# Performance work log

Measured on AMD Instinct MI355X. Metric: run time of the kernel, lower is better.

The kernel has to match this reference:

```python
import jax, jax.numpy as jnp
import numpy as np

N, K, C, SP = 65536, 16, 64, 8
C8 = C // SP  # attn_nn output dim == C // share_planes == 8
E = N * K
EPS = 1e-5


def _bn(x, g, b):
    # BatchNorm1d in training mode: batch statistics over the row dim
    mu = x.mean(0)
    var = ((x - mu) ** 2).mean(0)
    return (x - mu) * jax.lax.rsqrt(var + EPS) * g + b


def _segment_softmax(a, seg, n):
    m = jax.ops.segment_max(a, seg, num_segments=n)
    e = jnp.exp(a - m[seg])
    s = jax.ops.segment_sum(e, seg, num_segments=n)
    return e / s[seg]


def setup_inputs() -> dict:
    key = jax.random.key(0)
    ks = jax.random.split(key, 12)

    def w(k, shape, fan_in):
        return jax.random.normal(k, shape, jnp.float32) / np.sqrt(fan_in).astype(np.float32)

    x = jax.random.normal(ks[0], (N, C), jnp.float32)
    pos = jax.random.uniform(ks[1], (N, 3), jnp.float32)
    src = jax.random.randint(ks[2], (E,), 0, N)          # knn neighbor ids
    dst = jnp.repeat(jnp.arange(N), K)                   # k neighbors per target node
    edge_index = jnp.stack([src, dst]).astype(jnp.int32)
    return dict(
        x=x, pos=pos, edge_index=edge_index,
        W_in=w(ks[3], (C, C), C), W_out=w(ks[4], (C, C), C),
        pos_w1=w(ks[5], (3, 3), 3), pos_b1=jnp.zeros(3, jnp.float32),
        pos_bn_g=jnp.ones(3, jnp.float32), pos_bn_b=jnp.zeros(3, jnp.float32),
        pos_w2=w(ks[6], (C, 3), 3), pos_b2=jnp.zeros(C, jnp.float32),
        attn_bn1_g=jnp.ones(C, jnp.float32), attn_bn1_b=jnp.zeros(C, jnp.float32),
        attn_w1=w(ks[7], (C8, C), C), attn_b1=jnp.zeros(C8, jnp.float32),
        attn_bn2_g=jnp.ones(C8, jnp.float32), attn_bn2_b=jnp.zeros(C8, jnp.float32),
        attn_w2=w(ks[8], (C8, C8), C8), attn_b2=jnp.zeros(C8, jnp.float32),
        lin_w=w(ks[9], (C, C), C), lin_b=jnp.zeros(C, jnp.float32),
        src_w=w(ks[10], (C, C), C), src_b=jnp.zeros(C, jnp.float32),
        dst_w=w(ks[11], (C, C), C), dst_b=jnp.zeros(C, jnp.float32),
        bn1_g=jnp.ones(C, jnp.float32), bn1_b=jnp.zeros(C, jnp.float32),
        bn2_g=jnp.ones(C, jnp.float32), bn2_b=jnp.zeros(C, jnp.float32),
        bn3_g=jnp.ones(C, jnp.float32), bn3_b=jnp.zeros(C, jnp.float32),
    )


def reference(x, pos, edge_index, W_in, W_out, pos_w1, pos_b1, pos_bn_g, pos_bn_b,
              pos_w2, pos_b2, attn_bn1_g, attn_bn1_b, attn_w1, attn_b1,
              attn_bn2_g, attn_bn2_b, attn_w2, attn_b2, lin_w, lin_b,
              src_w, src_b, dst_w, dst_b, bn1_g, bn1_b, bn2_g, bn2_b, bn3_g, bn3_b):
    src, dst = edge_index[0], edge_index[1]
    x_skip = x
    # lin_in + bn1 + relu
    h = jax.nn.relu(_bn(x @ W_in.T, bn1_g, bn1_b))

    # --- PointTransformerConv ---
    a_src = h @ src_w.T + src_b
    a_dst = h @ dst_w.T + dst_b
    hW = h @ lin_w.T + lin_b

    rel = pos[src] - pos[dst]              # pos_j - pos_i  [E,3]
    d = jax.nn.relu(_bn(rel @ pos_w1.T + pos_b1, pos_bn_g, pos_bn_b))
    delta = d @ pos_w2.T + pos_b2          # [E,C]

    a = a_src[src] - a_dst[dst] + delta    # alpha_j - alpha_i + delta  [E,C]
    # attn_nn: BN -> ReLU -> (Lin C->C8, BN, ReLU) -> Lin C8->C8
    a = jax.nn.relu(_bn(a, attn_bn1_g, attn_bn1_b))
    a = jax.nn.relu(_bn(a @ attn_w1.T + attn_b1, attn_bn2_g, attn_bn2_b))
    a = a @ attn_w2.T + attn_b2            # [E,C8]
    alpha = _segment_softmax(a, dst, N)    # softmax over each node's neighborhood

    # grouped weighting with share_planes: [E,SP,C8] * [E,1,C8]
    msg = (alpha[:, None, :] * (hW[src] + delta).reshape(E, SP, C8)).reshape(E, C)
    out = jax.ops.segment_sum(msg, dst, num_segments=N)  # aggr='add'

    h2 = jax.nn.relu(_bn(out, bn2_g, bn2_b))
    h3 = _bn(h2 @ W_out.T, bn3_g, bn3_b)
    return jax.nn.relu(h3 + x_skip)
```

## Files before the change

### kernel.cpp

```cpp
#include <hip/hip_runtime.h>
#include <cstddef>

constexpr int N_ = 65536;
constexpr int K_ = 16;
constexpr int E_ = N_ * K_;
constexpr int C_ = 64;
#define EPS_ 1e-5f
#define SW 68
#define INV_N (1.f / 65536.f)
#define INV_E (1.f / 1048576.f)
#define NSLOT 64

typedef unsigned int uint_t;

__device__ __forceinline__ uint_t bf16_rne(float f) {
    uint_t u = __float_as_uint(f);
    return (u + 0x7fffu + ((u >> 16) & 1u)) >> 16;
}
__device__ __forceinline__ float bf16_lo(uint_t p) { return __uint_as_float(p << 16); }
__device__ __forceinline__ float bf16_hi(uint_t p) { return __uint_as_float(p & 0xffff0000u); }

__device__ __forceinline__ void bn_ss(const float* __restrict__ s, int nchp, int c,
                                      float invM, const float* __restrict__ g,
                                      const float* __restrict__ b,
                                      float& sc, float& sh)
{
    float mean = s[c] * invM;
    float var  = fmaxf(s[nchp + c] * invM - mean * mean, 0.f);
    sc = g[c] * rsqrtf(var + EPS_);
    sh = b[c] - mean * sc;
}

__global__ void k_zero(float* __restrict__ p, int n)
{
    int i = blockIdx.x * 1024 + threadIdx.x;
    if (i < n) p[i] = 0.f;
}

__device__ __forceinline__ void stage_x(const float* __restrict__ in,
                                        const float* __restrict__ ss,
                                        float* __restrict__ Xs, int row0, int t)
{
#pragma unroll
    for (int it = 0; it < 4; ++it) {
        int m = t + 256 * it;
        int r = m >> 4, j = m & 15;
        float4 v = ((const float4*)in)[(size_t)(row0 + r) * 16 + j];
        if (ss) {
            float4 sc = ((const float4*)ss)[j];
            float4 sh = ((const float4*)(ss + 64))[j];
            v.x = fmaxf(fmaf(v.x, sc.x, sh.x), 0.f);
            v.y = fmaxf(fmaf(v.y, sc.y, sh.y), 0.f);
            v.z = fmaxf(fmaf(v.z, sc.z, sh.z), 0.f);
            v.w = fmaxf(fmaf(v.w, sc.w, sh.w), 0.f);
        }
        *(float4*)&Xs[r * SW + 4 * j] = v;
    }
}

__device__ __forceinline__ void stage_w(const float* __restrict__ W,
                                        float* __restrict__ Ws, int t)
{
#pragma unroll
    for (int it = 0; it < 4; ++it) {
        int m = t + 256 * it;
        int r = m >> 4, j = m & 15;
        *(float4*)&Ws[r * SW + 4 * j] = ((const float4*)W)[m];
    }
}

__device__ __forceinline__ void compute_tile(const float* __restrict__ Xs,
                                             const float* __restrict__ Ws,
                                             int tx, int ty, float acc[4][4])
{
#pragma unroll
    for (int r = 0; r < 4; ++r)
#pragma unroll
        for (int c = 0; c < 4; ++c) acc[r][c] = 0.f;
    for (int kc = 0; kc < 16; ++kc) {
        float4 xf[4], wf[4];
#pragma unroll
        for (int r = 0; r < 4; ++r)
            xf[r] = *(const float4*)&Xs[(tx + 16 * r) * SW + 4 * kc];
#pragma unroll
        for (int c = 0; c < 4; ++c)
            wf[c] = *(const float4*)&Ws[(ty + 16 * c) * SW + 4 * kc];
#pragma unroll
        for (int r = 0; r < 4; ++r)
#pragma unroll
            for (int c = 0; c < 4; ++c) {
                acc[r][c] = fmaf(xf[r].x, wf[c].x, acc[r][c]);
                acc[r][c] = fmaf(xf[r].y, wf[c].y, acc[r][c]);
                acc[r][c] = fmaf(xf[r].z, wf[c].z, acc[r][c]);
                acc[r][c] = fmaf(xf[r].w, wf[c].w, acc[r][c]);
            }
    }
}

__device__ __forceinline__ void write_tile(float* __restrict__ buf, int tx, int ty,
                                           const float acc[4][4],
                                           const float* __restrict__ bias,
                                           float* __restrict__ out, int row0, int t)
{
    __syncthreads();
#pragma unroll
    for (int r = 0; r < 4; ++r)
#pragma unroll
        for (int c = 0; c < 4; ++c)
            buf[(tx + 16 * r) * SW + ty + 16 * c] = acc[r][c];
    __syncthreads();
#pragma unroll
    for (int it = 0; it < 4; ++it) {
        int m = t + 256 * it;
        int r = m >> 4, j = m & 15;
        float4 v = *(const float4*)&buf[r * SW + 4 * j];
        if (bias) {
            float4 bv = ((const float4*)bias)[j];
            v.x += bv.x; v.y += bv.y; v.z += bv.z; v.w += bv.w;
        }
        ((float4*)out)[(size_t)(row0 + r) * 16 + j] = v;
    }
    __syncthreads();
}

__device__ __forceinline__ void write_tile_bf16(float* __restrict__ buf, int tx, int ty,
                                                const float acc[4][4],
                                                const float* __restrict__ bias,
                                                unsigned short* __restrict__ out,
                                                int row0, int t)
{
    __syncthreads();
#pragma unroll
    for (int r = 0; r < 4; ++r)
#pragma unroll
        for (int c = 0; c < 4; ++c)
            buf[(tx + 16 * r) * SW + ty + 16 * c] = acc[r][c];
    __syncthreads();
#pragma unroll
    for (int it = 0; it < 4; ++it) {
        int m = t + 256 * it;
        int r = m >> 4, j = m & 15;
        float4 v = *(const float4*)&buf[r * SW + 4 * j];
        if (bias) {
            float4 bv = ((const float4*)bias)[j];
            v.x += bv.x; v.y += bv.y; v.z += bv.z; v.w += bv.w;
        }
        uint2 o;
        o.x = bf16_rne(v.x) | (bf16_rne(v.y) << 16);
        o.y = bf16_rne(v.z) | (bf16_rne(v.w) << 16);
        ((uint2*)out)[(size_t)(row0 + r) * 16 + j] = o;
    }
    __syncthreads();
}

__global__ __launch_bounds__(256)
void k_gemm_tile(const float* __restrict__ in, const float* __restrict__ W,
                 const float* __restrict__ acc_in, const float* __restrict__ g_in,
                 const float* __restrict__ b_in, float invM_in,
                 float* __restrict__ out, float* __restrict__ acc_out)
{
    __shared__ float Xs[64 * SW];
    __shared__ float Ws[64 * SW];
    __shared__ float ssm[128];
    __shared__ float raws[128];
    int t = threadIdx.x, tx = t & 15, ty = t >> 4;
    int row0 = blockIdx.x * 64;
    if (acc_in) {
        if (t < 128) {
            float s = 0.f;
            for (int sl = 0; sl < NSLOT; ++sl) s += acc_in[sl * 128 + t];
            raws[t] = s;
        }
        __syncthreads();
        if (t < 64) {
            float scv, shv;
            bn_ss(raws, 64, t, invM_in, g_in, b_in, scv, shv);
            ssm[t] = scv; ssm[64 + t] = shv;
        }
    }
    __syncthreads();
    stage_x(in, acc_in ? ssm : nullptr, Xs, row0, t);
    stage_w(W, Ws, t);
    __syncthreads();
    float acc[4][4];
    compute_tile(Xs, Ws, tx, ty, acc);
    __syncthreads();
#pragma unroll
    for (int r = 0; r < 4; ++r)
#pragma unroll
        for (int c = 0; c < 4; ++c)
            Ws[(tx + 16 * r) * SW + ty + 16 * c] = acc[r][c];
    __syncthreads();
    float s0 = 0, s1 = 0, s2 = 0, s3 = 0, q0 = 0, q1 = 0, q2 = 0, q3 = 0;
#pragma unroll
    for (int it = 0; it < 4; ++it) {
        int m = t + 256 * it;
        int r = m >> 4, j = m & 15;
        float4 v = *(const float4*)&Ws[r * SW + 4 * j];
        ((float4*)out)[(size_t)(row0 + r) * 16 + j] = v;
        s0 += v.x; q0 = fmaf(v.x, v.x, q0);
        s1 += v.y; q1 = fmaf(v.y, v.y, q1);
        s2 += v.z; q2 = fmaf(v.z, v.z, q2);
        s3 += v.w; q3 = fmaf(v.w, v.w, q3);
    }
    float4* scr = (float4*)Xs;
    scr[t]       = make_float4(s0, s1, s2, s3);
    scr[256 + t] = make_float4(q0, q1, q2, q3);
    __syncthreads();
    if (t < 16) {
        float4 S = make_float4(0, 0, 0, 0), Q = make_float4(0, 0, 0, 0);
#pragma unroll
        for (int k = 0; k < 16; ++k) {
            float4 a = scr[k * 16 + t], b = scr[256 + k * 16 + t];
            S.x += a.x; S.y += a.y; S.z += a.z; S.w += a.w;
            Q.x += b.x; Q.y += b.y; Q.z += b.z; Q.w += b.w;
        }
        float* ao = acc_out + (blockIdx.x & (NSLOT - 1)) * 128;
        atomicAdd(&ao[4 * t + 0], S.x); atomicAdd(&ao[4 * t + 1], S.y);
        atomicAdd(&ao[4 * t + 2], S.z); atomicAdd(&ao[4 * t + 3], S.w);
        atomicAdd(&ao[64 + 4 * t + 0], Q.x); atomicAdd(&ao[64 + 4 * t + 1], Q.y);
        atomicAdd(&ao[64 + 4 * t + 2], Q.z); atomicAdd(&ao[64 + 4 * t + 3], Q.w);
    }
}

__global__ __launch_bounds__(256)
void k_gemm3_tile(const float* __restrict__ y, const float* __restrict__ acc1,
                  const float* __restrict__ g1, const float* __restrict__ b1,
                  const float* __restrict__ Wa, const float* __restrict__ ba,
                  const float* __restrict__ Wb, const float* __restrict__ bb,
                  const float* __restrict__ Wc, const float* __restrict__ bc,
                  unsigned short* __restrict__ oa16, float* __restrict__ ob,
                  unsigned short* __restrict__ oc16)
{
    __shared__ float Xs[64 * SW];
    __shared__ float Ws[64 * SW];
    __shared__ float ssm[128];
    __shared__ float raws[128];
    int t = threadIdx.x, tx = t & 15, ty = t >> 4;
    int row0 = blockIdx.x * 64;
    if (t < 128) {
        float s = 0.f;
        for (int sl = 0; sl < NSLOT; ++sl) s += acc1[sl * 128 + t];
        raws[t] = s;
    }
    __syncthreads();
    if (t < 64) {
        float scv, shv;
        bn_ss(raws, 64, t, INV_N, g1, b1, scv, shv);
        ssm[t] = scv; ssm[64 + t] = shv;
    }
    __syncthreads();
    stage_x(y, ssm, Xs, row0, t);
    stage_w(Wa, Ws, t);
    __syncthreads();
    float acc[4][4];
    compute_tile(Xs, Ws, tx, ty, acc);
    write_tile_bf16(Ws, tx, ty, acc, ba, oa16, row0, t);
    stage_w(Wb, Ws, t);
    __syncthreads();
    compute_tile(Xs, Ws, tx, ty, acc);
    write_tile(Ws, tx, ty, acc, bb, ob, row0, t);
    stage_w(Wc, Ws, t);
    __syncthreads();
    compute_tile(Xs, Ws, tx, ty, acc);
    write_tile_bf16(Ws, tx, ty, acc, bc, oc16, row0, t);
}

__global__ __launch_bounds__(256)
void k_pos_stats(const float* __restrict__ pos, const int* __restrict__ src,
                 const float* __restrict__ pw1, const float* __restrict__ pb1,
                 float* __restrict__ acc)
{
    float s0 = 0, s1 = 0, s2 = 0, q0 = 0, q1 = 0, q2 = 0;
    int tid = blockIdx.x * 256 + threadIdx.x;
    for (int e = tid; e < E_; e += 1024 * 256) {
        int si = src[e], di = e >> 4;
        float rx = pos[3 * si + 0] - pos[3 * di + 0];
        float ry = pos[3 * si + 1] - pos[3 * di + 1];
        float rz = pos[3 * si + 2] - pos[3 * di + 2];
        float u0 = fmaf(rx, pw1[0], fmaf(ry, pw1[1], fmaf(rz, pw1[2], pb1[0])));
        float u1 = fmaf(rx, pw1[3], fmaf(ry, pw1[4], fmaf(rz, pw1[5], pb1[1])));
        float u2 = fmaf(rx, pw1[6], fmaf(ry, pw1[7], fmaf(rz, pw1[8], pb1[2])));
        s0 += u0; q0 = fmaf(u0, u0, q0);
        s1 += u1; q1 = fmaf(u1, u1, q1);
        s2 += u2; q2 = fmaf(u2, u2, q2);
    }
#pragma unroll
    for (int m = 1; m < 64; m <<= 1) {
        s0 += __shfl_xor(s0, m, 64); s1 += __shfl_xor(s1, m, 64); s2 += __shfl_xor(s2, m, 64);
        q0 += __shfl_xor(q0, m, 64); q1 += __shfl_xor(q1, m, 64); q2 += __shfl_xor(q2, m, 64);
    }
    __shared__ float red[4][8];
    int wv = threadIdx.x >> 6, ln = threadIdx.x & 63;
    if (ln == 0) {
        red[wv][0] = s0; red[wv][1] = s1; red[wv][2] = s2; red[wv][3] = 0.f;
        red[wv][4] = q0; red[wv][5] = q1; red[wv][6] = q2; red[wv][7] = 0.f;
    }
    __syncthreads();
    if (threadIdx.x < 8)
        atomicAdd(&acc[(blockIdx.x & (NSLOT - 1)) * 32 + threadIdx.x],
                  red[0][threadIdx.x] + red[1][threadIdx.x] + red[2][threadIdx.x] + red[3][threadIdx.x]);
}

__global__ __launch_bounds__(256)
void k_abn1_stats(const float* __restrict__ pos, const int* __restrict__ src,
                  const unsigned short* __restrict__ asrc16,
                  const float* __restrict__ adst,
                  const float* __restrict__ pw1, const float* __restrict__ pb1,
                  const float* __restrict__ accpos, const float* __restrict__ pbg,
                  const float* __restrict__ pbb, const float* __restrict__ pw2,
                  const float* __restrict__ pb2, float* __restrict__ acc_a1)
{
    __shared__ float rawP[8];
    int t = threadIdx.x;
    int l = t & 15, g = t >> 4, wv = t >> 6;
    int c0 = 4 * l;
    if (t < 8) {
        float s = 0.f;
        for (int sl = 0; sl < NSLOT; ++sl) s += accpos[sl * 32 + t];
        rawP[t] = s;
    }
    __syncthreads();
    float ps0, ph0, ps1, ph1, ps2, ph2;
    bn_ss(rawP, 4, 0, INV_E, pbg, pbb, ps0, ph0);
    bn_ss(rawP, 4, 1, INV_E, pbg, pbb, ps1, ph1);
    bn_ss(rawP, 4, 2, INV_E, pbg, pbb, ps2, ph2);
    float4 p0 = *(const float4*)(pw2 + 12 * l);
    float4 p1 = *(const float4*)(pw2 + 12 * l + 4);
    float4 p2 = *(const float4*)(pw2 + 12 * l + 8);
    float4 pb = *(const float4*)(pb2 + c0);
    float sa0 = 0, sa1 = 0, sa2 = 0, sa3 = 0;
    float qa0 = 0, qa1 = 0, qa2 = 0, qa3 = 0;
#pragma unroll
    for (int nn = 0; nn < 2; ++nn) {
        int n = blockIdx.x * 32 + nn * 16 + g;
        float4 dv = *(const float4*)(adst + (size_t)n * 64 + c0);
        float pnx = pos[3 * n + 0], pny = pos[3 * n + 1], pnz = pos[3 * n + 2];
        int si_l = src[n * 16 + l];
        float rx = pos[3 * si_l + 0] - pnx;
        float ry = pos[3 * si_l + 1] - pny;
        float rz = pos[3 * si_l + 2] - pnz;
        float u0 = fmaf(rx, pw1[0], fmaf(ry, pw1[1], fmaf(rz, pw1[2], pb1[0])));
        float u1 = fmaf(rx, pw1[3], fmaf(ry, pw1[4], fmaf(rz, pw1[5], pb1[1])));
        float u2 = fmaf(rx, pw1[6], fmaf(ry, pw1[7], fmaf(rz, pw1[8], pb1[2])));
        float dl0 = fmaxf(fmaf(u0, ps0, ph0), 0.f);
        float dl1 = fmaxf(fmaf(u1, ps1, ph1), 0.f);
        float dl2 = fmaxf(fmaf(u2, ps2, ph2), 0.f);
        for (int k = 0; k < 16; ++k) {
            int si = __shfl(si_l, k, 16);
            float d0 = __shfl(dl0, k, 16);
            float d1 = __shfl(dl1, k, 16);
            float d2 = __shfl(dl2, k, 16);
            uint2 raw = ((const uint2*)asrc16)[(size_t)si * 16 + l];
            float avx = bf16_lo(raw.x), avy = bf16_hi(raw.x);
            float avz = bf16_lo(raw.y), avw = bf16_hi(raw.y);
            float del0 = fmaf(d0, p0.x, fmaf(d1, p0.y, fmaf(d2, p0.z, pb.x)));
            float del1 = fmaf(d0, p0.w, fmaf(d1, p1.x, fmaf(d2, p1.y, pb.y)));
            float del2 = fmaf(d0, p1.z, fmaf(d1, p1.w, fmaf(d2, p2.x, pb.z)));
            float del3 = fmaf(d0, p2.y, fmaf(d1, p2.z, fmaf(d2, p2.w, pb.w)));
            float a0 = avx - dv.x + del0;
            float a1 = avy - dv.y + del1;
            float a2 = avz - dv.z + del2;
            float a3 = avw - dv.w + del3;
            sa0 += a0; qa0 = fmaf(a0, a0, qa0);
            sa1 += a1; qa1 = fmaf(a1, a1, qa1);
            sa2 += a2; qa2 = fmaf(a2, a2, qa2);
            sa3 += a3; qa3 = fmaf(a3, a3, qa3);
        }
    }
#pragma unroll
    for (int m = 16; m <= 32; m <<= 1) {
        sa0 += __shfl_xor(sa0, m, 64); sa1 += __shfl_xor(sa1, m, 64);
        sa2 += __shfl_xor(sa2, m, 64); sa3 += __shfl_xor(sa3, m, 64);
        qa0 += __shfl_xor(qa0, m, 64); qa1 += __shfl_xor(qa1, m, 64);
        qa2 += __shfl_xor(qa2, m, 64); qa3 += __shfl_xor(qa3, m, 64);
    }
    __shared__ float red[4][128];
    if ((t & 63) < 16) {
        red[wv][c0 + 0] = sa0; red[wv][c0 + 1] = sa1;
        red[wv][c0 + 2] = sa2; red[wv][c0 + 3] = sa3;
        red[wv][64 + c0 + 0] = qa0; red[wv][64 + c0 + 1] = qa1;
        red[wv][64 + c0 + 2] = qa2; red[wv][64 + c0 + 3] = qa3;
    }
    __syncthreads();
    if (t < 128)
        atomicAdd(&acc_a1[(blockIdx.x & (NSLOT - 1)) * 128 + t],
                  red[0][t] + red[1][t] + red[2][t] + red[3][t]);
}

__global__ __launch_bounds__(256)
void k_edge_t1(const float* __restrict__ pos, const int* __restrict__ src,
               const unsigned short* __restrict__ asrc16,
               const float* __restrict__ adst,
               const float* __restrict__ pw1, const float* __restrict__ pb1,
               const float* __restrict__ accpos, const float* __restrict__ pbg,
               const float* __restrict__ pbb, const float* __restrict__ pw2,
               const float* __restrict__ pb2, const float* __restrict__ acc_a1,
               const float* __restrict__ a1g, const float* __restrict__ a1b,
               const float* __restrict__ aw1, const float* __restrict__ ab1,
               float* __restrict__ t1, float* __restrict__ acc_a2)
{
    __shared__ float rawA1[128];
    __shared__ float rawP[8];
    int t = threadIdx.x;
    int l = t & 15, g = t >> 4, wv = t >> 6;
    int c0 = 4 * l;
    int ch = 4 * (l & 1) + 2 * ((l >> 1) & 1) + ((l >> 2) & 1);
    float abv = ab1[ch];
    if (t < 128) {
        float s = 0.f;
        for (int sl = 0; sl < NSLOT; ++sl) s += acc_a1[sl * 128 + t];
        rawA1[t] = s;
    } else if (t < 136) {
        int i = t - 128;
        float s = 0.f;
        for (int sl = 0; sl < NSLOT; ++sl) s += accpos[sl * 32 + i];
        rawP[i] = s;
    }
    __syncthreads();
    float ps0, ph0, ps1, ph1, ps2, ph2;
    bn_ss(rawP, 4, 0, INV_E, pbg, pbb, ps0, ph0);
    bn_ss(rawP, 4, 1, INV_E, pbg, pbb, ps1, ph1);
    bn_ss(rawP, 4, 2, INV_E, pbg, pbb, ps2, ph2);
    float scx, shx, scy, shy, scz, shz, scw, shw;
    bn_ss(rawA1, 64, c0 + 0, INV_E, a1g, a1b, scx, shx);
    bn_ss(rawA1, 64, c0 + 1, INV_E, a1g, a1b, scy, shy);
    bn_ss(rawA1, 64, c0 + 2, INV_E, a1g, a1b, scz, shz);
    bn_ss(rawA1, 64, c0 + 3, INV_E, a1g, a1b, scw, shw);
    float4 p0 = *(const float4*)(pw2 + 12 * l);
    float4 p1 = *(const float4*)(pw2 + 12 * l + 4);
    float4 p2 = *(const float4*)(pw2 + 12 * l + 8);
    float4 pb = *(const float4*)(pb2 + c0);
    float4 w1[8];
#pragma unroll
    for (int jj = 0; jj < 8; ++jj) w1[jj] = *(const float4*)(aw1 + jj * 64 + c0);
    float sse = 0.f, ssq = 0.f;
#pragma unroll
    for (int nn = 0; nn < 2; ++nn) {
        int n = blockIdx.x * 32 + nn * 16 + g;
        float4 dv = *(const float4*)(adst + (size_t)n * 64 + c0);
        float pnx = pos[3 * n + 0], pny = pos[3 * n + 1], pnz = pos[3 * n + 2];
        int si_l = src[n * 16 + l];
        float rx = pos[3 * si_l + 0] - pnx;
        float ry = pos[3 * si_l + 1] - pny;
        float rz = pos[3 * si_l + 2] - pnz;
        float u0 = fmaf(rx, pw1[0], fmaf(ry, pw1[1], fmaf(rz, pw1[2], pb1[0])));
        float u1 = fmaf(rx, pw1[3], fmaf(ry, pw1[4], fmaf(rz, pw1[5], pb1[1])));
        float u2 = fmaf(rx, pw1[6], fmaf(ry, pw1[7], fmaf(rz, pw1[8], pb1[2])));
        float dl0 = fmaxf(fmaf(u0, ps0, ph0), 0.f);
        float dl1 = fmaxf(fmaf(u1, ps1, ph1), 0.f);
        float dl2 = fmaxf(fmaf(u2, ps2, ph2), 0.f);
        for (int k = 0; k < 16; ++k) {
            int si = __shfl(si_l, k, 16);
            float d0 = __shfl(dl0, k, 16);
            float d1 = __shfl(dl1, k, 16);
            float d2 = __shfl(dl2, k, 16);
            uint2 raw = ((const uint2*)asrc16)[(size_t)si * 16 + l];
            float avx = bf16_lo(raw.x), avy = bf16_hi(raw.x);
            float avz = bf16_lo(raw.y), avw = bf16_hi(raw.y);
            float del0 = fmaf(d0, p0.x, fmaf(d1, p0.y, fmaf(d2, p0.z, pb.x)));
            float del1 = fmaf(d0, p0.w, fmaf(d1, p1.x, fmaf(d2, p1.y, pb.y)));
            float del2 = fmaf(d0, p1.z, fmaf(d1, p1.w, fmaf(d2, p2.x, pb.z)));
            float del3 = fmaf(d0, p2.y, fmaf(d1, p2.z, fmaf(d2, p2.w, pb.w)));
            float an0 = fmaxf(fmaf(avx - dv.x + del0, scx, shx), 0.f);
            float an1 = fmaxf(fmaf(avy - dv.y + del1, scy, shy), 0.f);
            float an2 = fmaxf(fmaf(avz - dv.z + del2, scz, shz), 0.f);
            float an3 = fmaxf(fmaf(avw - dv.w + del3, scw, shw), 0.f);
            float tp[8];
#pragma unroll
            for (int jj = 0; jj < 8; ++jj)
                tp[jj] = fmaf(an0, w1[jj].x, fmaf(an1, w1[jj].y,
                         fmaf(an2, w1[jj].z, an3 * w1[jj].w)));
            float s4[4];
#pragma unroll
            for (int j = 0; j < 4; ++j) {
                float send = (l & 1) ? tp[j] : tp[j + 4];
                float recv = __shfl_xor(send, 1, 64);
                s4[j] = ((l & 1) ? tp[j + 4] : tp[j]) + recv;
            }
            float s2[2];
#pragma unroll
            for (int j = 0; j < 2; ++j) {
                float send = (l & 2) ? s4[j] : s4[j + 2];
                float recv = __shfl_xor(send, 2, 64);
                s2[j] = ((l & 2) ? s4[j + 2] : s4[j]) + recv;
            }
            float send = (l & 4) ? s2[0] : s2[1];
            float recv = __shfl_xor(send, 4, 64);
            float s1 = ((l & 4) ? s2[1] : s2[0]) + recv;
            s1 += __shfl_xor(s1, 8, 64);
            float o = s1 + abv;
            if (l < 8) t1[(size_t)(n * 16 + k) * 8 + ch] = o;
            sse += o; ssq = fmaf(o, o, ssq);
        }
    }
#pragma unroll
    for (int m = 16; m <= 32; m <<= 1) {
        sse += __shfl_xor(sse, m, 64);
        ssq += __shfl_xor(ssq, m, 64);
    }
    __shared__ float red[4][16];
    if ((t & 63) < 8) { red[wv][ch] = sse; red[wv][8 + ch] = ssq; }
    __syncthreads();
    if (t < 16)
        atomicAdd(&acc_a2[(blockIdx.x & (NSLOT - 1)) * 32 + t],
                  red[0][t] + red[1][t] + red[2][t] + red[3][t]);
}

__global__ __launch_bounds__(256)
void k_node_aggr(const float* __restrict__ pos, const int* __restrict__ src,
                 const float* __restrict__ t1, const float* __restrict__ acc_a2,
                 const float* __restrict__ a2g, const float* __restrict__ a2b,
                 const float* __restrict__ aw2, const float* __restrict__ ab2,
                 const unsigned short* __restrict__ hw16,
                 const float* __restrict__ accpos, const float* __restrict__ pbg,
                 const float* __restrict__ pbb,
                 const float* __restrict__ pw1, const float* __restrict__ pb1,
                 const float* __restrict__ pw2, const float* __restrict__ pb2,
                 float* __restrict__ out, float* __restrict__ acc_bn2)
{
    __shared__ float alds[16][196];
    __shared__ float ssm2[16];
    __shared__ float rawA2[16];
    __shared__ float rawP[8];
    int t = threadIdx.x, l = t & 15, g = t >> 4;
    int c0 = 4 * l;
    if (t < 16) {
        float s = 0.f;
        for (int sl = 0; sl < NSLOT; ++sl) s += acc_a2[sl * 32 + t];
        rawA2[t] = s;
    } else if (t < 24) {
        int i = t - 16;
        float s = 0.f;
        for (int sl = 0; sl < NSLOT; ++sl) s += accpos[sl * 32 + i];
        rawP[i] = s;
    }
    __syncthreads();
    if (t < 8) {
        float scv, shv;
        bn_ss(rawA2, 8, t, INV_E, a2g, a2b, scv, shv);
        ssm2[t] = scv; ssm2[8 + t] = shv;
    }
    __syncthreads();
    float ps0, ph0, ps1, ph1, ps2, ph2;
    bn_ss(rawP, 4, 0, INV_E, pbg, pbb, ps0, ph0);
    bn_ss(rawP, 4, 1, INV_E, pbg, pbb, ps1, ph1);
    bn_ss(rawP, 4, 2, INV_E, pbg, pbb, ps2, ph2);
    float4 p0 = *(const float4*)(pw2 + 12 * l);
    float4 p1 = *(const float4*)(pw2 + 12 * l + 4);
    float4 p2 = *(const float4*)(pw2 + 12 * l + 8);
    float4 pb = *(const float4*)(pb2 + c0);
    int alof = (l & 1) * 4;
    int n = blockIdx.x * 16 + g;
    int e = n * 16 + l;
    const float4* t4 = (const float4*)(t1 + (size_t)e * 8);
    float4 ta = t4[0], tb = t4[1];
    float tv[8] = {ta.x, ta.y, ta.z, ta.w, tb.x, tb.y, tb.z, tb.w};
    float tn[8];
#pragma unroll
    for (int j = 0; j < 8; ++j)
        tn[j] = fmaxf(fmaf(tv[j], ssm2[j], ssm2[8 + j]), 0.f);
    float al[8];
#pragma unroll
    for (int j = 0; j < 8; ++j) {
        float acc = ab2[j];
#pragma unroll
        for (int i = 0; i < 8; ++i) acc = fmaf(tn[i], aw2[j * 8 + i], acc);
        float m = acc;
#pragma unroll
        for (int msk = 1; msk < 16; msk <<= 1) m = fmaxf(m, __shfl_xor(m, msk, 64));
        float ex = __expf(acc - m);
        float sm = ex;
#pragma unroll
        for (int msk = 1; msk < 16; msk <<= 1) sm += __shfl_xor(sm, msk, 64);
        al[j] = ex / sm;
    }
    *(float4*)&alds[g][l * 12]     = make_float4(al[0], al[1], al[2], al[3]);
    *(float4*)&alds[g][l * 12 + 4] = make_float4(al[4], al[5], al[6], al[7]);
    int silane = src[e];
    float pnx = pos[3 * n + 0], pny = pos[3 * n + 1], pnz = pos[3 * n + 2];
    float rx = pos[3 * silane + 0] - pnx;
    float ry = pos[3 * silane + 1] - pny;
    float rz = pos[3 * silane + 2] - pnz;
    float u0 = fmaf(rx, pw1[0], fmaf(ry, pw1[1], fmaf(rz, pw1[2], pb1[0])));
    float u1 = fmaf(rx, pw1[3], fmaf(ry, pw1[4], fmaf(rz, pw1[5], pb1[1])));
    float u2 = fmaf(rx, pw1[6], fmaf(ry, pw1[7], fmaf(rz, pw1[8], pb1[2])));
    float dl0 = fmaxf(fmaf(u0, ps0, ph0), 0.f);
    float dl1 = fmaxf(fmaf(u1, ps1, ph1), 0.f);
    float dl2 = fmaxf(fmaf(u2, ps2, ph2), 0.f);
    float a0 = 0.f, a1 = 0.f, a2 = 0.f, a3 = 0.f;
#pragma unroll 4
    for (int k = 0; k < 16; ++k) {
        int sk = __shfl(silane, k, 16);
        float d0 = __shfl(dl0, k, 16);
        float d1 = __shfl(dl1, k, 16);
        float d2 = __shfl(dl2, k, 16);
        uint2 raw = ((const uint2*)hw16)[(size_t)sk * 16 + l];
        float hvx = bf16_lo(raw.x), hvy = bf16_hi(raw.x);
        float hvz = bf16_lo(raw.y), hvw = bf16_hi(raw.y);
        float4 alv = *(const float4*)&alds[g][k * 12 + alof];
        float del0 = fmaf(d0, p0.x, fmaf(d1, p0.y, fmaf(d2, p0.z, pb.x)));
        float del1 = fmaf(d0, p0.w, fmaf(d1, p1.x, fmaf(d2, p1.y, pb.y)));
        float del2 = fmaf(d0, p1.z, fmaf(d1, p1.w, fmaf(d2, p2.x, pb.z)));
        float del3 = fmaf(d0, p2.y, fmaf(d1, p2.z, fmaf(d2, p2.w, pb.w)));
        a0 = fmaf(alv.x, hvx + del0, a0);
        a1 = fmaf(alv.y, hvy + del1, a1);
        a2 = fmaf(alv.z, hvz + del2, a2);
        a3 = fmaf(alv.w, hvw + del3, a3);
    }
    *(float4*)(out + (size_t)n * 64 + c0) = make_float4(a0, a1, a2, a3);
    __syncthreads();
    float4* scr = (float4*)&alds[0][0];
    scr[g * 16 + l]       = make_float4(a0, a1, a2, a3);
    scr[256 + g * 16 + l] = make_float4(a0 * a0, a1 * a1, a2 * a2, a3 * a3);
    __syncthreads();
    if (t < 16) {
        float4 S = make_float4(0, 0, 0, 0), Q = make_float4(0, 0, 0, 0);
#pragma unroll
        for (int k = 0; k < 16; ++k) {
            float4 a = scr[k * 16 + t], b = scr[256 + k * 16 + t];
            S.x += a.x; S.y += a.y; S.z += a.z; S.w += a.w;
            Q.x += b.x; Q.y += b.y; Q.z += b.z; Q.w += b.w;
        }
        float* ao = acc_bn2 + (blockIdx.x & (NSLOT - 1)) * 128;
        atomicAdd(&ao[4 * t + 0], S.x); atomicAdd(&ao[4 * t + 1], S.y);
        atomicAdd(&ao[4 * t + 2], S.z); atomicAdd(&ao[4 * t + 3], S.w);
        atomicAdd(&ao[64 + 4 * t + 0], Q.x); atomicAdd(&ao[64 + 4 * t + 1], Q.y);
        atomicAdd(&ao[64 + 4 * t + 2], Q.z); atomicAdd(&ao[64 + 4 * t + 3], Q.w);
    }
}

__global__ __launch_bounds__(256)
void k_final(const float* __restrict__ y3, const float* __restrict__ acc3,
             const float* __restrict__ g3, const float* __restrict__ b3,
             const float* __restrict__ x, float* __restrict__ out)
{
    __shared__ float raws[128];
    __shared__ float ssl[128];
    int t = threadIdx.x;
    if (t < 128) {
        float s = 0.f;
        for (int sl = 0; sl < NSLOT; ++sl) s += acc3[sl * 128 + t];
        raws[t] = s;
    }
    __syncthreads();
    if (t < 64) {
        float scv, shv;
        bn_ss(raws, 64, t, INV_N, g3, b3, scv, shv);
        ssl[t] = scv; ssl[64 + t] = shv;
    }
    __syncthreads();
    int i = blockIdx.x * 256 + t;
    int c4 = i & 15;
    float4 sc = *(const float4*)&ssl[4 * c4];
    float4 sh = *(const float4*)&ssl[64 + 4 * c4];
    float4 v  = ((const float4*)y3)[i];
    float4 xs = ((const float4*)x)[i];
    float4 o;
    o.x = fmaxf(fmaf(v.x, sc.x, sh.x) + xs.x, 0.f);
    o.y = fmaxf(fmaf(v.y, sc.y, sh.y) + xs.y, 0.f);
    o.z = fmaxf(fmaf(v.z, sc.z, sh.z) + xs.z, 0.f);
    o.w = fmaxf(fmaf(v.w, sc.w, sh.w) + xs.w, 0.f);
    ((float4*)out)[i] = o;
}

extern "C" void kernel_launch(void* const* d_in, const int* in_sizes, int n_in,
                              void* d_out, int out_size, void* d_ws, size_t ws_size,
                              hipStream_t stream)
{
    const float* x    = (const float*)d_in[0];
    const float* pos  = (const float*)d_in[1];
    const int*   src  = (const int*)d_in[2];
    const float* W_in = (const float*)d_in[3];
    const float* W_out= (const float*)d_in[4];
    const float* pw1  = (const float*)d_in[5];
    const float* pb1  = (const float*)d_in[6];
    const float* pbg  = (const float*)d_in[7];
    const float* pbb  = (const float*)d_in[8];
    const float* pw2  = (const float*)d_in[9];
    const float* pb2  = (const float*)d_in[10];
    const float* a1g  = (const float*)d_in[11];
    const float* a1b  = (const float*)d_in[12];
    const float* aw1  = (const float*)d_in[13];
    const float* ab1  = (const float*)d_in[14];
    const float* a2g  = (const float*)d_in[15];
    const float* a2b  = (const float*)d_in[16];
    const float* aw2  = (const float*)d_in[17];
    const float* ab2  = (const float*)d_in[18];
    const float* linw = (const float*)d_in[19];
    const float* linb = (const float*)d_in[20];
    const float* srcw = (const float*)d_in[21];
    const float* srcb = (const float*)d_in[22];
    const float* dstw = (const float*)d_in[23];
    const float* dstb = (const float*)d_in[24];
    const float* bn1g = (const float*)d_in[25];
    const float* bn1b = (const float*)d_in[26];
    const float* bn2g = (const float*)d_in[27];
    const float* bn2b = (const float*)d_in[28];
    const float* bn3g = (const float*)d_in[29];
    const float* bn3b = (const float*)d_in[30];
    float* outp = (float*)d_out;

    float* ws = (float*)d_ws;
    const size_t NC = (size_t)N_ * C_;
    float* buf_y     = ws;
    float* buf_adst  = ws + NC;
    unsigned short* asrc16 = (unsigned short*)(ws + 2 * NC);
    unsigned short* hw16   = (unsigned short*)(ws + 2 * NC + NC / 2);
    float* buf_t1    = ws + 3 * NC;
    float* accb      = ws + 3 * NC + (size_t)E_ * 8;
    float* acc_bn1 = accb;
    float* acc_pos = accb + 64 * 128;
    float* acc_a1  = acc_pos + 64 * 32;
    float* acc_a2  = acc_a1 + 64 * 128;
    float* acc_bn2 = acc_a2 + 64 * 32;
    float* acc_bn3 = acc_bn2 + 64 * 128;
    const int ACC_TOTAL = 64 * (128 + 32 + 128 + 32 + 128 + 128);
    float* buf_out = buf_adst;

    k_zero<<<(ACC_TOTAL + 1023) / 1024, 1024, 0, stream>>>(accb, ACC_TOTAL);
    k_gemm_tile<<<1024, 256, 0, stream>>>(x, W_in, nullptr, nullptr, nullptr, 0.f,
                                          buf_y, acc_bn1);
    k_gemm3_tile<<<1024, 256, 0, stream>>>(buf_y, acc_bn1, bn1g, bn1b,
                                           srcw, srcb, dstw, dstb, linw, linb,
                                           asrc16, buf_adst, hw16);
    k_pos_stats<<<1024, 256, 0, stream>>>(pos, src, pw1, pb1, acc_pos);
    k_abn1_stats<<<2048, 256, 0, stream>>>(pos, src, asrc16, buf_adst,
                                           pw1, pb1, acc_pos, pbg, pbb,
                                           pw2, pb2, acc_a1);
    k_edge_t1<<<2048, 256, 0, stream>>>(pos, src, asrc16, buf_adst,
                                        pw1, pb1, acc_pos, pbg, pbb, pw2, pb2,
                                        acc_a1, a1g, a1b, aw1, ab1,
                                        buf_t1, acc_a2);
    k_node_aggr<<<4096, 256, 0, stream>>>(pos, src, buf_t1, acc_a2, a2g, a2b,
                                          aw2, ab2, hw16, acc_pos, pbg, pbb,
                                          pw1, pb1, pw2, pb2, buf_out, acc_bn2);
    k_gemm_tile<<<1024, 256, 0, stream>>>(buf_out, W_out, acc_bn2, bn2g, bn2b, INV_N,
                                          buf_y, acc_bn3);
    k_final<<<(N_ * C_ / 4) / 256, 256, 0, stream>>>(buf_y, acc_bn3, bn3g, bn3b, x, outp);

    (void)in_sizes; (void)n_in; (void)out_size; (void)ws_size;
}
```

Measured before the change: 327.1 us.

## Compute attn_w1 projection in edge kernel with bf16 MFMA via LDS staging

Replaces the per-lane FMA dot products and shuffle-based butterfly reduction for the 64->8 attention projection with a bf16 MFMA 16x16x32. Normalized activations are packed to bf16 and written to a swizzled LDS tile, then each wave loads its A fragments and multiplies them against bf16-packed attn_w1 columns held in registers. This removes many FMAs and cross-lane shuffles per edge, but adds bf16 rounding of both activations and weights, a 32KB LDS buffer that may reduce occupancy, and a fully unrolled k loop. There is no barrier between the LDS writes and reads; this looks safe only because each wave reads rows its own lanes wrote.

```diff
diff --git a/kernel.cpp b/kernel.cpp
--- a/kernel.cpp
+++ b/kernel.cpp
@@ -12,6 +12,8 @@
 #define NSLOT 64
 
 typedef unsigned int uint_t;
+typedef float f32x4_t __attribute__((ext_vector_type(4)));
+typedef short bf16x8_t __attribute__((ext_vector_type(8)));
 
 __device__ __forceinline__ uint_t bf16_rne(float f) {
     uint_t u = __float_as_uint(f);
@@ -19,6 +21,9 @@
 }
 __device__ __forceinline__ float bf16_lo(uint_t p) { return __uint_as_float(p << 16); }
 __device__ __forceinline__ float bf16_hi(uint_t p) { return __uint_as_float(p & 0xffff0000u); }
+__device__ __forceinline__ uint_t pk2(float a, float b) {
+    return bf16_rne(a) | (bf16_rne(b) << 16);
+}
 
 __device__ __forceinline__ void bn_ss(const float* __restrict__ s, int nchp, int c,
                                       float invM, const float* __restrict__ g,
@@ -400,13 +405,14 @@
                const float* __restrict__ aw1, const float* __restrict__ ab1,
                float* __restrict__ t1, float* __restrict__ acc_a2)
 {
+    __shared__ uint2 an_lds[4096];
     __shared__ float rawA1[128];
     __shared__ float rawP[8];
+    __shared__ float red[4][16];
     int t = threadIdx.x;
     int l = t & 15, g = t >> 4, wv = t >> 6;
+    int L = t & 63;
     int c0 = 4 * l;
-    int ch = 4 * (l & 1) + 2 * ((l >> 1) & 1) + ((l >> 2) & 1);
-    float abv = ab1[ch];
     if (t < 128) {
         float s = 0.f;
         for (int sl = 0; sl < NSLOT; ++sl) s += acc_a1[sl * 128 + t];
@@ -431,10 +437,24 @@
     float4 p1 = *(const float4*)(pw2 + 12 * l + 4);
     float4 p2 = *(const float4*)(pw2 + 12 * l + 8);
     float4 pb = *(const float4*)(pb2 + c0);
-    float4 w1[8];
-#pragma unroll
-    for (int jj = 0; jj < 8; ++jj) w1[jj] = *(const float4*)(aw1 + jj * 64 + c0);
-    float sse = 0.f, ssq = 0.f;
+    int col = L & 15, kb = L >> 4;
+    uint4 bf0 = make_uint4(0u, 0u, 0u, 0u);
+    uint4 bf1 = make_uint4(0u, 0u, 0u, 0u);
+    float biasc = 0.f;
+    if (col < 8) {
+        const float* wr = aw1 + col * 64 + kb * 8;
+        bf0 = make_uint4(pk2(wr[0], wr[1]), pk2(wr[2], wr[3]),
+                         pk2(wr[4], wr[5]), pk2(wr[6], wr[7]));
+        const float* wr2 = wr + 32;
+        bf1 = make_uint4(pk2(wr2[0], wr2[1]), pk2(wr2[2], wr2[3]),
+                         pk2(wr2[4], wr2[5]), pk2(wr2[6], wr2[7]));
+        biasc = ab1[col];
+    }
+    int ar = col;
+    int aoff0 = ar * 128 + ((kb * 16) ^ ((ar & 7) << 4));
+    int aoff1 = ar * 128 + ((64 + kb * 16) ^ ((ar & 7) << 4));
+    char* anb = (char*)an_lds;
+    float se = 0.f, sq = 0.f;
 #pragma unroll
     for (int nn = 0; nn < 2; ++nn) {
         int n = blockIdx.x * 32 + nn * 16 + g;
@@ -450,6 +470,7 @@
         float dl0 = fmaxf(fmaf(u0, ps0, ph0), 0.f);
         float dl1 = fmaxf(fmaf(u1, ps1, ph1), 0.f);
         float dl2 = fmaxf(fmaf(u2, ps2, ph2), 0.f);
+#pragma unroll
         for (int k = 0; k < 16; ++k) {
             int si = __shfl(si_l, k, 16);
             float d0 = __shfl(dl0, k, 16);
@@ -466,41 +487,35 @@
             float an1 = fmaxf(fmaf(avy - dv.y + del1, scy, shy), 0.f);
             float an2 = fmaxf(fmaf(avz - dv.z + del2, scz, shz), 0.f);
             float an3 = fmaxf(fmaf(avw - dv.w + del3, scw, shw), 0.f);
-            float tp[8];
-#pragma unroll
-            for (int jj = 0; jj < 8; ++jj)
-                tp[jj] = fmaf(an0, w1[jj].x, fmaf(an1, w1[jj].y,
-                         fmaf(an2, w1[jj].z, an3 * w1[jj].w)));
-            float s4[4];
-#pragma unroll
-            for (int j = 0; j < 4; ++j) {
-                float send = (l & 1) ? tp[j] : tp[j + 4];
-                float recv = __shfl_xor(send, 1, 64);
-                s4[j] = ((l & 1) ? tp[j + 4] : tp[j]) + recv;
+            int woff = g * 2048 + k * 128 + ((8 * l) ^ ((k & 7) << 4));
+            *(uint2*)(anb + woff) = make_uint2(pk2(an0, an1), pk2(an2, an3));
+        }
+#pragma unroll
+        for (int tt = 0; tt < 4; ++tt) {
+            int g2 = (wv << 2) + tt;
+            int tb = g2 * 2048;
+            uint4 a0 = *(const uint4*)(anb + tb + aoff0);
+            uint4 a1v = *(const uint4*)(anb + tb + aoff1);
+            f32x4_t acc = {0.f, 0.f, 0.f, 0.f};
+            acc = __builtin_amdgcn_mfma_f32_16x16x32_bf16(
+                      *(const bf16x8_t*)&a0, *(const bf16x8_t*)&bf0, acc, 0, 0, 0);
+            acc = __builtin_amdgcn_mfma_f32_16x16x32_bf16(
+                      *(const bf16x8_t*)&a1v, *(const bf16x8_t*)&bf1, acc, 0, 0, 0);
+            if (col < 8) {
+                int n2 = blockIdx.x * 32 + nn * 16 + g2;
+                float* op = t1 + (size_t)(n2 * 16 + kb * 4) * 8 + col;
+#pragma unroll
+                for (int j = 0; j < 4; ++j) {
+                    float v = acc[j] + biasc;
+                    op[j * 8] = v;
+                    se += v; sq = fmaf(v, v, sq);
+                }
             }
-            float s2[2];
-#pragma unroll
-            for (int j = 0; j < 2; ++j) {
-                float send = (l & 2) ? s4[j] : s4[j + 2];
-                float recv = __shfl_xor(send, 2, 64);
-                s2[j] = ((l & 2) ? s4[j + 2] : s4[j]) + recv;
-            }
-            float send = (l & 4) ? s2[0] : s2[1];
-            float recv = __shfl_xor(send, 4, 64);
-            float s1 = ((l & 4) ? s2[1] : s2[0]) + recv;
-            s1 += __shfl_xor(s1, 8, 64);
-            float o = s1 + abv;
-            if (l < 8) t1[(size_t)(n * 16 + k) * 8 + ch] = o;
-            sse += o; ssq = fmaf(o, o, ssq);
-        }
-    }
-#pragma unroll
-    for (int m = 16; m <= 32; m <<= 1) {
-        sse += __shfl_xor(sse, m, 64);
-        ssq += __shfl_xor(ssq, m, 64);
-    }
-    __shared__ float red[4][16];
-    if ((t & 63) < 8) { red[wv][ch] = sse; red[wv][8 + ch] = ssq; }
+        }
+    }
+    se += __shfl_xor(se, 16, 64); sq += __shfl_xor(sq, 16, 64);
+    se += __shfl_xor(se, 32, 64); sq += __shfl_xor(sq, 32, 64);
+    if (L < 8) { red[wv][col] = se; red[wv][8 + col] = sq; }
     __syncthreads();
     if (t < 16)
         atomicAdd(&acc_a2[(blockIdx.x & (NSLOT - 1)) * 32 + t],
```

After: 321.5 us. Within noise of the previous version (-1.7%).
